# Optimization experiments

Measured on AMD Instinct MI355X. Metric: run time of the kernel, lower is better.

The kernel has to match this reference:

```python
import jax, jax.numpy as jnp
import numpy as np

EPS = 1e-12

def _l2norm(v, axis=-1):
    n = jnp.sqrt(jnp.sum(v * v, axis=axis, keepdims=True))
    return v / jnp.maximum(n, EPS)

def setup_inputs() -> dict:
    key = jax.random.key(0)
    ks = jax.random.split(key, 6)
    B, S, E, A = 256, 128, 768, 30
    x = jax.random.normal(ks[0], (B, S, E), dtype=jnp.float32)
    W_att = jax.random.normal(ks[1], (E, E), dtype=jnp.float32) * (1.0 / np.sqrt(E))
    b_att = jnp.zeros((E,), dtype=jnp.float32)
    W_red = jax.random.normal(ks[2], (E, A), dtype=jnp.float32) * (1.0 / np.sqrt(E))
    b_red = jnp.zeros((A,), dtype=jnp.float32)
    aspect_W = jax.random.normal(ks[3], (A, E), dtype=jnp.float32) * (1.0 / np.sqrt(E))
    # negatives: uniform over other batch elements (multinomial on ones - eye)
    idx = jax.random.randint(ks[4], (B, 10), 0, B - 1)
    neg_idx = (idx + (idx >= jnp.arange(B)[:, None])).astype(jnp.int32)  # skip self
    return {"x": x, "W_att": W_att, "b_att": b_att, "W_red": W_red,
            "b_red": b_red, "aspect_W": aspect_W, "neg_idx": neg_idx}

def reference(x, W_att, b_att, W_red, b_red, aspect_W, neg_idx):
    # --- LuongAttention(general): query = mean over seq ---
    q = x.mean(axis=1)                                   # [B,E]
    qW = q @ W_att + b_att                               # [B,E]
    scores = jnp.einsum('bse,be->bs', x, qW)             # [B,S]
    attn = jax.nn.softmax(scores, axis=-1)
    z_s = jnp.einsum('bs,bse->be', attn, x)              # attended sentence vec [B,E]
    # --- reduction + reconstruction ---
    composition = jax.nn.softmax(z_s @ W_red + b_red, axis=-1)  # [B,A]
    reconstructed = composition @ aspect_W                      # [B,E]
    # --- max-margin loss with gathered negatives ---
    r_s = _l2norm(reconstructed)                         # F.normalize
    z_n = z_s[neg_idx]                                   # [B,10,E] gather
    pos = jnp.einsum('be,be->b', z_s, r_s)[:, None]      # [B,1]
    negs = jnp.einsum('bne,be->bn', z_n, r_s)            # [B,10]
    J = 1.0 - pos + negs
    margin_loss = jnp.mean(jnp.maximum(J, 0.0))
    # --- orthogonal regularization on aspect embeddings ---
    T_n = _l2norm(aspect_W, axis=1)                      # [A,E]
    G = T_n @ T_n.T - jnp.eye(aspect_W.shape[0], dtype=aspect_W.dtype)
    reg = jnp.sqrt(jnp.sum(G * G))                       # Frobenius norm
    loss = reg + margin_loss
    return (z_s, reconstructed, loss)
```

## Files before the change

### kernel.cpp

```cpp
#include <hip/hip_runtime.h>
#include <hip/hip_bf16.h>
#include <hip/hip_fp16.h>
#include <math.h>

#define B 256
#define S 128
#define E 768
#define E4 192
#define NA 30
#define NNEG 10

#define K2_KC 96

__device__ __forceinline__ float dot4(float4 a, float4 b) {
    return a.x * b.x + a.y * b.y + a.z * b.z + a.w * b.w;
}
__device__ __forceinline__ float wave_reduce_sum(float v) {
#pragma unroll
    for (int off = 32; off; off >>= 1) v += __shfl_down(v, off);
    return v;
}
__device__ __forceinline__ float wave_reduce_max(float v) {
#pragma unroll
    for (int off = 32; off; off >>= 1) v = fmaxf(v, __shfl_down(v, off));
    return v;
}
__device__ __forceinline__ float4 h4_to_f4(uint2 p) {
    __half2* ph = (__half2*)&p;
    float2 f0 = __half22float2(ph[0]);
    float2 f1 = __half22float2(ph[1]);
    return make_float4(f0.x, f0.y, f1.x, f1.y);
}

template <int USE16>
__global__ __launch_bounds__(768) void mean_prep_kernel(const float* __restrict__ x,
                                                        const float* __restrict__ W_red,
                                                        const float* __restrict__ aspect_W,
                                                        float* __restrict__ q,
                                                        float* __restrict__ WredT,
                                                        float* __restrict__ invn,
                                                        __half* __restrict__ xh) {
    int bid = blockIdx.x;
    int tid = threadIdx.x;
    __shared__ __align__(16) float4 part[4][E4];
    __shared__ float red[12];

    if (bid < 2 * B) {
        int b = bid >> 1, half = bid & 1;
        int c = tid % E4;
        int g = tid / E4;
        const float4* xb = (const float4*)(x + (size_t)b * S * E);
        uint2* xhb = (uint2*)(xh + (size_t)b * S * E);
        int s0 = half * 64 + g * 16;
        float4 acc = make_float4(0.f, 0.f, 0.f, 0.f);
#pragma unroll 4
        for (int s = s0; s < s0 + 16; ++s) {
            float4 v = xb[(size_t)s * E4 + c];
            acc.x += v.x; acc.y += v.y; acc.z += v.z; acc.w += v.w;
            if (USE16) {
                __half2 h01 = __floats2half2_rn(v.x, v.y);
                __half2 h23 = __floats2half2_rn(v.z, v.w);
                uint2 pk;
                pk.x = *(unsigned int*)&h01;
                pk.y = *(unsigned int*)&h23;
                xhb[(size_t)s * E4 + c] = pk;
            }
        }
        part[g][c] = acc;
        __syncthreads();
        if (tid < E4) {
            float4 a0 = part[0][c], a1 = part[1][c], a2 = part[2][c], a3 = part[3][c];
            const float inv = 1.0f / (float)S;
            float4 r;
            r.x = (a0.x + a1.x + a2.x + a3.x) * inv;
            r.y = (a0.y + a1.y + a2.y + a3.y) * inv;
            r.z = (a0.z + a1.z + a2.z + a3.z) * inv;
            r.w = (a0.w + a1.w + a2.w + a3.w) * inv;
            ((float4*)q)[((size_t)half * B + b) * E4 + c] = r;
        }
    } else {
        int a = bid - 2 * B;
        WredT[(size_t)a * E + tid] = W_red[(size_t)tid * NA + a];
        int wave = tid >> 6, lane = tid & 63;
        float v = aspect_W[(size_t)a * E + tid];
        float ss = wave_reduce_sum(v * v);
        if (lane == 0) red[wave] = ss;
        __syncthreads();
        if (tid == 0) {
            float n = 0.f;
#pragma unroll
            for (int w = 0; w < 12; ++w) n += red[w];
            invn[a] = 1.0f / fmaxf(sqrtf(n), 1e-12f);
        }
    }
}

__global__ __launch_bounds__(256) void qw_partial_kernel(const float* __restrict__ q,
                                                         const float* __restrict__ W_att,
                                                         float* __restrict__ part) {
    int b0 = blockIdx.x * 64;
    int e0 = blockIdx.y * 64;
    int kz = blockIdx.z;
    int k0 = kz * K2_KC;
    int tid = threadIdx.x;

    __shared__ __align__(16) float qs[64][K2_KC + 4];
    __shared__ __align__(16) float ws[K2_KC][64];

    int r0 = (tid >> 3) * 2;
    int c0 = (tid & 7) * 8;

    float4 a00 = make_float4(0,0,0,0), a01 = make_float4(0,0,0,0);
    float4 a10 = make_float4(0,0,0,0), a11 = make_float4(0,0,0,0);

    {
        int row = tid >> 2, ks = (tid & 3) * 24;
        const float* src0 = q + (size_t)(b0 + row) * E + k0 + ks;
        const float* src1 = src0 + (size_t)B * E;
#pragma unroll
        for (int j = 0; j < 6; ++j) {
            float4 v0 = *(const float4*)(src0 + 4 * j);
            float4 v1 = *(const float4*)(src1 + 4 * j);
            v0.x += v1.x; v0.y += v1.y; v0.z += v1.z; v0.w += v1.w;
            *(float4*)&qs[row][ks + 4 * j] = v0;
        }
    }
    for (int i = tid; i < K2_KC * 16; i += 256) {
        int row = i >> 4, e4 = (i & 15) * 4;
        *(float4*)&ws[row][e4] =
            *(const float4*)(W_att + (size_t)(k0 + row) * E + e0 + e4);
    }
    __syncthreads();
#pragma unroll 4
    for (int k = 0; k < K2_KC; ++k) {
        float qa = qs[r0][k], qb = qs[r0 + 1][k];
        float4 w0 = *(const float4*)&ws[k][c0];
        float4 w1 = *(const float4*)&ws[k][c0 + 4];
        a00.x += qa * w0.x; a00.y += qa * w0.y; a00.z += qa * w0.z; a00.w += qa * w0.w;
        a01.x += qa * w1.x; a01.y += qa * w1.y; a01.z += qa * w1.z; a01.w += qa * w1.w;
        a10.x += qb * w0.x; a10.y += qb * w0.y; a10.z += qb * w0.z; a10.w += qb * w0.w;
        a11.x += qb * w1.x; a11.y += qb * w1.y; a11.z += qb * w1.z; a11.w += qb * w1.w;
    }
    float* dst = part + ((size_t)kz * B + b0 + r0) * E + e0 + c0;
    *(float4*)dst = a00; *(float4*)(dst + 4) = a01;
    *(float4*)(dst + E) = a10; *(float4*)(dst + E + 4) = a11;
}

template <int USE16>
__global__ __launch_bounds__(512) void attn_ortho_kernel(const float* __restrict__ x,
                                                         const __half* __restrict__ xh,
                                                         const float* __restrict__ part,
                                                         const float* __restrict__ b_att,
                                                         const float* __restrict__ aspect_W,
                                                         const float* __restrict__ invn,
                                                         float* __restrict__ z_s,
                                                         float* __restrict__ Gpart) {
    int bid = blockIdx.x;
    int tid = threadIdx.x, wave = tid >> 6, lane = tid & 63;
    __shared__ __align__(16) float4 qw4[E4];
    __shared__ __align__(16) float4 zw[8][E4];
    __shared__ float wm[8], wl[8];
    __shared__ float red[8];

    if (bid >= B) {
        int i = bid - B;
        float inv_i = invn[i];
        if (tid < E4) {
            float4 v = ((const float4*)aspect_W)[(size_t)i * E4 + tid];
            v.x *= inv_i; v.y *= inv_i; v.z *= inv_i; v.w *= inv_i;
            qw4[tid] = v;
        }
        __syncthreads();
        float acc = 0.f;
        for (int j = wave; j < NA; j += 8) {
            const float4* aj = (const float4*)(aspect_W + (size_t)j * E);
            float d = 0.f;
#pragma unroll
            for (int jj = 0; jj < 3; ++jj)
                d += dot4(aj[lane + 64 * jj], qw4[lane + 64 * jj]);
            d = wave_reduce_sum(d);
            if (lane == 0) {
                float g = d * invn[j] - ((i == j) ? 1.f : 0.f);
                acc += g * g;
            }
        }
        if (lane == 0) red[wave] = acc;
        __syncthreads();
        if (tid == 0) {
            float s = 0.f;
#pragma unroll
            for (int w = 0; w < 8; ++w) s += red[w];
            Gpart[i] = s;
        }
        return;
    }

    int b = bid;
    const int N4 = B * E / 4;
    if (tid < E4) {
        const float4* p = (const float4*)part;
        size_t base = (size_t)b * E4 + tid;
        float4 r = ((const float4*)b_att)[tid];
#pragma unroll
        for (int i = 0; i < 8; ++i) {
            float4 s = p[base + (size_t)i * N4];
            r.x += s.x; r.y += s.y; r.z += s.z; r.w += s.w;
        }
        qw4[tid] = r;
    }
    __syncthreads();

    float4 q0 = qw4[lane], q1 = qw4[lane + 64], q2 = qw4[lane + 128];

    float m0 = -3.4e38f, l0 = 0.f, m1 = -3.4e38f, l1 = 0.f;
    float4 p00 = make_float4(0.f,0.f,0.f,0.f), p01 = p00, p02 = p00;
    float4 p10 = p00, p11 = p00, p12 = p00;

    const uint2*  xhb = (const uint2*)(xh + (size_t)b * S * E);
    const float4* xb  = (const float4*)(x + (size_t)b * S * E);
    int s0 = wave * 16;

#pragma unroll
    for (int i = 0; i < 16; i += 4) {
        float4 xA0, xA1, xA2, xB0, xB1, xB2, xC0, xC1, xC2, xD0, xD1, xD2;
        if (USE16) {
            const uint2* rA = xhb + (size_t)(s0 + i) * E4;
            const uint2* rB = rA + E4;
            const uint2* rC = rB + E4;
            const uint2* rD = rC + E4;
            xA0 = h4_to_f4(rA[lane]); xA1 = h4_to_f4(rA[lane + 64]); xA2 = h4_to_f4(rA[lane + 128]);
            xB0 = h4_to_f4(rB[lane]); xB1 = h4_to_f4(rB[lane + 64]); xB2 = h4_to_f4(rB[lane + 128]);
            xC0 = h4_to_f4(rC[lane]); xC1 = h4_to_f4(rC[lane + 64]); xC2 = h4_to_f4(rC[lane + 128]);
            xD0 = h4_to_f4(rD[lane]); xD1 = h4_to_f4(rD[lane + 64]); xD2 = h4_to_f4(rD[lane + 128]);
        } else {
            const float4* rA = xb + (size_t)(s0 + i) * E4;
            const float4* rB = rA + E4;
            const float4* rC = rB + E4;
            const float4* rD = rC + E4;
            xA0 = rA[lane]; xA1 = rA[lane + 64]; xA2 = rA[lane + 128];
            xB0 = rB[lane]; xB1 = rB[lane + 64]; xB2 = rB[lane + 128];
            xC0 = rC[lane]; xC1 = rC[lane + 64]; xC2 = rC[lane + 128];
            xD0 = rD[lane]; xD1 = rD[lane + 64]; xD2 = rD[lane + 128];
        }
        float dA = dot4(xA0, q0) + dot4(xA1, q1) + dot4(xA2, q2);
        float dB = dot4(xB0, q0) + dot4(xB1, q1) + dot4(xB2, q2);
        float dC = dot4(xC0, q0) + dot4(xC1, q1) + dot4(xC2, q2);
        float dD = dot4(xD0, q0) + dot4(xD1, q1) + dot4(xD2, q2);
#pragma unroll
        for (int off = 32; off; off >>= 1) {
            dA += __shfl_xor(dA, off);
            dB += __shfl_xor(dB, off);
            dC += __shfl_xor(dC, off);
            dD += __shfl_xor(dD, off);
        }
        float tm0 = fmaxf(m0, fmaxf(dA, dB));
        float sc0 = __expf(m0 - tm0);
        float eA = __expf(dA - tm0), eB = __expf(dB - tm0);
        float tm1 = fmaxf(m1, fmaxf(dC, dD));
        float sc1 = __expf(m1 - tm1);
        float eC = __expf(dC - tm1), eD = __expf(dD - tm1);

        l0 = l0 * sc0 + eA + eB;
        l1 = l1 * sc1 + eC + eD;
        p00.x = p00.x * sc0 + eA * xA0.x + eB * xB0.x;
        p00.y = p00.y * sc0 + eA * xA0.y + eB * xB0.y;
        p00.z = p00.z * sc0 + eA * xA0.z + eB * xB0.z;
        p00.w = p00.w * sc0 + eA * xA0.w + eB * xB0.w;
        p10.x = p10.x * sc1 + eC * xC0.x + eD * xD0.x;
        p10.y = p10.y * sc1 + eC * xC0.y + eD * xD0.y;
        p10.z = p10.z * sc1 + eC * xC0.z + eD * xD0.z;
        p10.w = p10.w * sc1 + eC * xC0.w + eD * xD0.w;
        p01.x = p01.x * sc0 + eA * xA1.x + eB * xB1.x;
        p01.y = p01.y * sc0 + eA * xA1.y + eB * xB1.y;
        p01.z = p01.z * sc0 + eA * xA1.z + eB * xB1.z;
        p01.w = p01.w * sc0 + eA * xA1.w + eB * xB1.w;
        p11.x = p11.x * sc1 + eC * xC1.x + eD * xD1.x;
        p11.y = p11.y * sc1 + eC * xC1.y + eD * xD1.y;
        p11.z = p11.z * sc1 + eC * xC1.z + eD * xD1.z;
        p11.w = p11.w * sc1 + eC * xC1.w + eD * xD1.w;
        p02.x = p02.x * sc0 + eA * xA2.x + eB * xB2.x;
        p02.y = p02.y * sc0 + eA * xA2.y + eB * xB2.y;
        p02.z = p02.z * sc0 + eA * xA2.z + eB * xB2.z;
        p02.w = p02.w * sc0 + eA * xA2.w + eB * xB2.w;
        p12.x = p12.x * sc1 + eC * xC2.x + eD * xD2.x;
        p12.y = p12.y * sc1 + eC * xC2.y + eD * xD2.y;
        p12.z = p12.z * sc1 + eC * xC2.z + eD * xD2.z;
        p12.w = p12.w * sc1 + eC * xC2.w + eD * xD2.w;
        m0 = tm0;
        m1 = tm1;
    }

    float m = fmaxf(m0, m1);
    float f0 = __expf(m0 - m), f1 = __expf(m1 - m);
    float l = l0 * f0 + l1 * f1;
    float4 a0, a1, a2;
    a0.x = p00.x * f0 + p10.x * f1; a0.y = p00.y * f0 + p10.y * f1;
    a0.z = p00.z * f0 + p10.z * f1; a0.w = p00.w * f0 + p10.w * f1;
    a1.x = p01.x * f0 + p11.x * f1; a1.y = p01.y * f0 + p11.y * f1;
    a1.z = p01.z * f0 + p11.z * f1; a1.w = p01.w * f0 + p11.w * f1;
    a2.x = p02.x * f0 + p12.x * f1; a2.y = p02.y * f0 + p12.y * f1;
    a2.z = p02.z * f0 + p12.z * f1; a2.w = p02.w * f0 + p12.w * f1;

    zw[wave][lane] = a0;
    zw[wave][lane + 64] = a1;
    zw[wave][lane + 128] = a2;
    if (lane == 0) { wm[wave] = m; wl[wave] = l; }
    __syncthreads();

    if (tid < E4) {
        float M = wm[0];
#pragma unroll
        for (int w = 1; w < 8; ++w) M = fmaxf(M, wm[w]);
        float L = 0.f;
        float4 z = make_float4(0.f, 0.f, 0.f, 0.f);
#pragma unroll
        for (int w = 0; w < 8; ++w) {
            float f = __expf(wm[w] - M);
            float4 a = zw[w][tid];
            z.x += f * a.x; z.y += f * a.y; z.z += f * a.z; z.w += f * a.w;
            L += f * wl[w];
        }
        float invL = 1.0f / L;
        z.x *= invL; z.y *= invL; z.z *= invL; z.w *= invL;
        ((float4*)z_s)[(size_t)b * E4 + tid] = z;
    }
}

__global__ __launch_bounds__(768) void recon_margin_kernel(const float* __restrict__ z_s,
                                                           const float* __restrict__ WredT,
                                                           const float* __restrict__ b_red,
                                                           const float* __restrict__ aspect_W,
                                                           const int* __restrict__ neg_idx,
                                                           float* __restrict__ recon,
                                                           float* __restrict__ mpart) {
    int b = blockIdx.x;
    int tid = threadIdx.x, wave = tid >> 6, lane = tid & 63;
    __shared__ __align__(16) float4 z4[E4];
    __shared__ float comp[NA];
    __shared__ __align__(16) float r_sh[E];
    __shared__ float red[12];
    __shared__ float dots[12];

    if (tid < E4) z4[tid] = ((const float4*)(z_s + (size_t)b * E))[tid];
    __syncthreads();

    for (int a = wave; a < NA; a += 12) {
        const float4* wr = (const float4*)(WredT + (size_t)a * E);
        float d = 0.f;
#pragma unroll
        for (int j = 0; j < 3; ++j)
            d += dot4(wr[lane + 64 * j], z4[lane + 64 * j]);
        d = wave_reduce_sum(d);
        if (lane == 0) comp[a] = d + b_red[a];
    }
    __syncthreads();

    if (wave == 0) {
        float v = (lane < NA) ? comp[lane] : -3.4e38f;
        float m = wave_reduce_max(v);
        m = __shfl(m, 0);
        float e = (lane < NA) ? expf(v - m) : 0.f;
        float ssum = wave_reduce_sum(e);
        ssum = __shfl(ssum, 0);
        if (lane < NA) comp[lane] = e / ssum;
    }
    __syncthreads();

    float r = 0.f;
    for (int a = 0; a < NA; ++a)
        r += comp[a] * aspect_W[(size_t)a * E + tid];
    recon[(size_t)b * E + tid] = r;
    r_sh[tid] = r;
    float sq = wave_reduce_sum(r * r);
    if (lane == 0) red[wave] = sq;
    __syncthreads();
    float tot = 0.f;
#pragma unroll
    for (int w = 0; w < 12; ++w) tot += red[w];
    float inv = 1.0f / fmaxf(sqrtf(tot), 1e-12f);

    if (wave <= NNEG) {
        int row = (wave == 0) ? b : neg_idx[b * NNEG + (wave - 1)];
        const float4* zr = (const float4*)(z_s + (size_t)row * E);
        const float4* rr = (const float4*)r_sh;
        float acc = 0.f;
#pragma unroll
        for (int j = 0; j < 3; ++j)
            acc += dot4(zr[lane + 64 * j], rr[lane + 64 * j]);
        acc = wave_reduce_sum(acc);
        if (lane == 0) dots[wave] = acc;
    }
    __syncthreads();
    if (tid == 0) {
        float pos = dots[0] * inv;
        float ssum = 0.f;
        for (int n = 1; n <= NNEG; ++n)
            ssum += fmaxf(1.f - pos + dots[n] * inv, 0.f);
        mpart[b] = ssum;
    }
}

__global__ __launch_bounds__(256) void loss_kernel(const float* __restrict__ Gpart,
                                                   const float* __restrict__ mpart,
                                                   float* __restrict__ loss_out) {
    int tid = threadIdx.x, wave = tid >> 6, lane = tid & 63;
    __shared__ float ra[4], rb[4];
    float fr = (tid < NA) ? Gpart[tid] : 0.f;
    fr = wave_reduce_sum(fr);
    if (lane == 0) ra[wave] = fr;
    float mp = mpart[tid];
    mp = wave_reduce_sum(mp);
    if (lane == 0) rb[wave] = mp;
    __syncthreads();
    if (tid == 0) {
        float frob = sqrtf(ra[0] + ra[1] + ra[2] + ra[3]);
        float msum = rb[0] + rb[1] + rb[2] + rb[3];
        loss_out[0] = frob + msum * (1.0f / (float)(B * NNEG));
    }
}

extern "C" void kernel_launch(void* const* d_in, const int* in_sizes, int n_in,
                              void* d_out, int out_size, void* d_ws, size_t ws_size,
                              hipStream_t stream) {
    const float* x        = (const float*)d_in[0];
    const float* W_att    = (const float*)d_in[1];
    const float* b_att    = (const float*)d_in[2];
    const float* W_red    = (const float*)d_in[3];
    const float* b_red    = (const float*)d_in[4];
    const float* aspect_W = (const float*)d_in[5];
    const int*   neg_idx  = (const int*)d_in[6];

    float* out   = (float*)d_out;
    float* z_s   = out;
    float* recon = out + (size_t)B * E;
    float* loss  = out + (size_t)2 * B * E;

    float* ws    = (float*)d_ws;
    float* q     = ws;
    float* part2 = q + (size_t)2 * B * E;
    float* WredT = part2 + (size_t)8 * B * E;
    float* invn  = WredT + (size_t)NA * E;
    float* Gpart = invn + 32;
    float* mpart = Gpart + 32;
    float* endf  = mpart + B;

    size_t base_floats = (size_t)(endf - ws);
    size_t need = base_floats * sizeof(float) + (size_t)B * S * E * sizeof(__half);
    bool use16 = (ws_size >= need);
    __half* xh = (__half*)(ws + base_floats);

    if (use16) {
        mean_prep_kernel<1><<<2 * B + NA, 768, 0, stream>>>(x, W_red, aspect_W, q, WredT, invn, xh);
        qw_partial_kernel<<<dim3(4, 12, 8), 256, 0, stream>>>(q, W_att, part2);
        attn_ortho_kernel<1><<<B + NA, 512, 0, stream>>>(x, xh, part2, b_att, aspect_W, invn, z_s, Gpart);
    } else {
        mean_prep_kernel<0><<<2 * B + NA, 768, 0, stream>>>(x, W_red, aspect_W, q, WredT, invn, xh);
        qw_partial_kernel<<<dim3(4, 12, 8), 256, 0, stream>>>(q, W_att, part2);
        attn_ortho_kernel<0><<<B + NA, 512, 0, stream>>>(x, xh, part2, b_att, aspect_W, invn, z_s, Gpart);
    }
    recon_margin_kernel<<<B, 768, 0, stream>>>(z_s, WredT, b_red, aspect_W, neg_idx, recon, mpart);
    loss_kernel<<<1, 256, 0, stream>>>(Gpart, mpart, loss);
}
```

Baseline: 64.20 us.

## Split attention over sequence halves with a separate combine kernel

The attention kernel now launches two blocks per batch row. Each block handles 64 sequence positions and writes an unnormalized partial z together with its max and sum. A new small kernel merges the two halves with the log-sum-exp rescaling and writes z_s. The goal is to double the block count so the GPU's compute units are better occupied. The cost is an extra kernel launch, a second global round trip for the partial z vectors, and the qW reduction over 8 partials being repeated in both blocks.

```diff
diff --git a/kernel.cpp b/kernel.cpp
--- a/kernel.cpp
+++ b/kernel.cpp
@@ -147,14 +147,16 @@
 }
 
 template <int USE16>
-__global__ __launch_bounds__(512) void attn_ortho_kernel(const float* __restrict__ x,
-                                                         const __half* __restrict__ xh,
-                                                         const float* __restrict__ part,
-                                                         const float* __restrict__ b_att,
-                                                         const float* __restrict__ aspect_W,
-                                                         const float* __restrict__ invn,
-                                                         float* __restrict__ z_s,
-                                                         float* __restrict__ Gpart) {
+__global__ __launch_bounds__(512) void attn_half_kernel(const float* __restrict__ x,
+                                                        const __half* __restrict__ xh,
+                                                        const float* __restrict__ part,
+                                                        const float* __restrict__ b_att,
+                                                        const float* __restrict__ aspect_W,
+                                                        const float* __restrict__ invn,
+                                                        float* __restrict__ zhalf,
+                                                        float* __restrict__ mh,
+                                                        float* __restrict__ lh,
+                                                        float* __restrict__ Gpart) {
     int bid = blockIdx.x;
     int tid = threadIdx.x, wave = tid >> 6, lane = tid & 63;
     __shared__ __align__(16) float4 qw4[E4];
@@ -162,8 +164,8 @@
     __shared__ float wm[8], wl[8];
     __shared__ float red[8];
 
-    if (bid >= B) {
-        int i = bid - B;
+    if (bid >= 2 * B) {
+        int i = bid - 2 * B;
         float inv_i = invn[i];
         if (tid < E4) {
             float4 v = ((const float4*)aspect_W)[(size_t)i * E4 + tid];
@@ -195,7 +197,7 @@
         return;
     }
 
-    int b = bid;
+    int b = bid >> 1, h = bid & 1;
     const int N4 = B * E / 4;
     if (tid < E4) {
         const float4* p = (const float4*)part;
@@ -218,10 +220,10 @@
 
     const uint2*  xhb = (const uint2*)(xh + (size_t)b * S * E);
     const float4* xb  = (const float4*)(x + (size_t)b * S * E);
-    int s0 = wave * 16;
-
-#pragma unroll
-    for (int i = 0; i < 16; i += 4) {
+    int s0 = h * 64 + wave * 8;
+
+#pragma unroll
+    for (int i = 0; i < 8; i += 4) {
         float4 xA0, xA1, xA2, xB0, xB1, xB2, xC0, xC1, xC2, xD0, xD1, xD2;
         if (USE16) {
             const uint2* rA = xhb + (size_t)(s0 + i) * E4;
@@ -320,10 +322,30 @@
             z.x += f * a.x; z.y += f * a.y; z.z += f * a.z; z.w += f * a.w;
             L += f * wl[w];
         }
-        float invL = 1.0f / L;
-        z.x *= invL; z.y *= invL; z.z *= invL; z.w *= invL;
-        ((float4*)z_s)[(size_t)b * E4 + tid] = z;
-    }
+        ((float4*)zhalf)[(size_t)bid * E4 + tid] = z;
+        if (tid == 0) { mh[bid] = M; lh[bid] = L; }
+    }
+}
+
+__global__ __launch_bounds__(192) void zcombine_kernel(const float* __restrict__ zhalf,
+                                                       const float* __restrict__ mh,
+                                                       const float* __restrict__ lh,
+                                                       float* __restrict__ z_s) {
+    int b = blockIdx.x;
+    int tid = threadIdx.x;
+    float m0 = mh[2 * b], m1 = mh[2 * b + 1];
+    float M = fmaxf(m0, m1);
+    float f0 = __expf(m0 - M), f1 = __expf(m1 - M);
+    float L = f0 * lh[2 * b] + f1 * lh[2 * b + 1];
+    float invL = 1.0f / L;
+    float4 z0 = ((const float4*)zhalf)[(size_t)(2 * b) * E4 + tid];
+    float4 z1 = ((const float4*)zhalf)[(size_t)(2 * b + 1) * E4 + tid];
+    float4 z;
+    z.x = (f0 * z0.x + f1 * z1.x) * invL;
+    z.y = (f0 * z0.y + f1 * z1.y) * invL;
+    z.z = (f0 * z0.z + f1 * z1.z) * invL;
+    z.w = (f0 * z0.w + f1 * z1.w) * invL;
+    ((float4*)z_s)[(size_t)b * E4 + tid] = z;
 }
 
 __global__ __launch_bounds__(768) void recon_margin_kernel(const float* __restrict__ z_s,
@@ -442,7 +464,10 @@
     float* invn  = WredT + (size_t)NA * E;
     float* Gpart = invn + 32;
     float* mpart = Gpart + 32;
-    float* endf  = mpart + B;
+    float* zhalf = mpart + B;
+    float* mh    = zhalf + (size_t)2 * B * E;
+    float* lhv   = mh + 2 * B;
+    float* endf  = lhv + 2 * B;
 
     size_t base_floats = (size_t)(endf - ws);
     size_t need = base_floats * sizeof(float) + (size_t)B * S * E * sizeof(__half);
@@ -452,12 +477,15 @@
     if (use16) {
         mean_prep_kernel<1><<<2 * B + NA, 768, 0, stream>>>(x, W_red, aspect_W, q, WredT, invn, xh);
         qw_partial_kernel<<<dim3(4, 12, 8), 256, 0, stream>>>(q, W_att, part2);
-        attn_ortho_kernel<1><<<B + NA, 512, 0, stream>>>(x, xh, part2, b_att, aspect_W, invn, z_s, Gpart);
+        attn_half_kernel<1><<<2 * B + NA, 512, 0, stream>>>(x, xh, part2, b_att, aspect_W, invn,
+                                                            zhalf, mh, lhv, Gpart);
     } else {
         mean_prep_kernel<0><<<2 * B + NA, 768, 0, stream>>>(x, W_red, aspect_W, q, WredT, invn, xh);
         qw_partial_kernel<<<dim3(4, 12, 8), 256, 0, stream>>>(q, W_att, part2);
-        attn_ortho_kernel<0><<<B + NA, 512, 0, stream>>>(x, xh, part2, b_att, aspect_W, invn, z_s, Gpart);
-    }
+        attn_half_kernel<0><<<2 * B + NA, 512, 0, stream>>>(x, xh, part2, b_att, aspect_W, invn,
+                                                            zhalf, mh, lhv, Gpart);
+    }
+    zcombine_kernel<<<B, 192, 0, stream>>>(zhalf, mh, lhv, z_s);
     recon_margin_kernel<<<B, 768, 0, stream>>>(z_s, WredT, b_red, aspect_W, neg_idx, recon, mpart);
     loss_kernel<<<1, 256, 0, stream>>>(Gpart, mpart, loss);
 }
```

Result: slower. 67.14 us (+4.6%).
